# Performance work log

Hardware: AMD Instinct MI355X
Metric: run time of the kernel (lower is better)

## Reference

```python
import jax, jax.numpy as jnp
import numpy as np

B, H, W, C = 8, 64, 64, 512
DQK = C // 8  # query/key channel dim from Conv2D(filters//8, 1)


def setup_inputs() -> dict:
    key = jax.random.key(0)
    ks = jax.random.split(key, 8)
    s_in = 1.0 / np.sqrt(C)
    x = jax.random.normal(ks[0], (B, H, W, C), dtype=jnp.float32)
    Wq = jax.random.normal(ks[1], (C, DQK), dtype=jnp.float32) * s_in
    bq = jnp.zeros((DQK,), dtype=jnp.float32)
    Wk = jax.random.normal(ks[2], (C, DQK), dtype=jnp.float32) * s_in
    bk = jnp.zeros((DQK,), dtype=jnp.float32)
    Wv = jax.random.normal(ks[3], (C, C), dtype=jnp.float32) * s_in
    bv = jnp.zeros((C,), dtype=jnp.float32)
    # gamma initialized to zeros in the original, but use a nonzero value so
    # the attention branch actually contributes to the output/gradients.
    gamma = jnp.ones((1,), dtype=jnp.float32) * 0.5
    return {"x": x, "Wq": Wq, "bq": bq, "Wk": Wk, "bk": bk,
            "Wv": Wv, "bv": bv, "gamma": gamma}


def reference(x, Wq, bq, Wk, bk, Wv, bv, gamma):
    b, h, w, c = x.shape
    n = h * w  # spatial_size
    xf = x.reshape(b, n, c)
    # 1x1 convs == per-pixel channel matmuls
    q = xf @ Wq + bq            # [B, N, C//8]
    k = xf @ Wk + bk            # [B, N, C//8]
    v = xf @ Wv + bv            # [B, N, C]
    # Dot(axes=-1): attn[b,i,j] = sum_d q[b,i,d] * k[b,j,d]
    attn = jnp.einsum('bid,bjd->bij', q, k)
    attn = jax.nn.softmax(attn, axis=-1)
    # Dot(axes=-2): out[b,j,c] = sum_i attn[b,i,j] * v[b,i,c]  (note transpose)
    out = jnp.einsum('bij,bic->bjc', attn, v)
    out = out.reshape(b, h, w, c)
    return gamma * out + x
```

## Files before the change

### kernel.cpp

```cpp
#include <hip/hip_runtime.h>
#include <hip/hip_bf16.h>
#include <cstdio>

typedef unsigned short u16;
typedef __attribute__((ext_vector_type(4))) float f32x4;
typedef __attribute__((ext_vector_type(8))) short s16x8;

#define LOG2E 1.4426950408889634f

__device__ __forceinline__ u16 bf16b(float f) {
  union { float f; unsigned u; } c; c.f = f;
  unsigned u = c.u;
  return (u16)((u + 0x7FFFu + ((u >> 16) & 1u)) >> 16);
}

__device__ __forceinline__ void load16(const void* g, void* l) {
  __builtin_amdgcn_global_load_lds(
      (const __attribute__((address_space(1))) void*)g,
      (__attribute__((address_space(3))) void*)l, 16, 0, 0);
}


__global__ __launch_bounds__(256) void cvt_all_k(const float* __restrict__ x,
                                                 const float* __restrict__ Wq,
                                                 const float* __restrict__ Wk,
                                                 const float* __restrict__ Wv,
                                                 u16* __restrict__ xb,
                                                 u16* __restrict__ Wcat) {
  int bid = blockIdx.x;
  if (bid < 16384) {
    long i = ((long)bid * 256 + threadIdx.x) * 4;
    float4 f = *(const float4*)&x[i];
    unsigned lo = (unsigned)bf16b(f.x) | ((unsigned)bf16b(f.y) << 16);
    unsigned hi = (unsigned)bf16b(f.z) | ((unsigned)bf16b(f.w) << 16);
    uint2 v; v.x = lo; v.y = hi;
    *(uint2*)&xb[i] = v;
  } else {
    int idx = (bid - 16384) * 256 + threadIdx.x;
    int nn = idx >> 9, k = idx & 511;
    float v;
    if (nn < 64)       v = Wq[k * 64 + nn];
    else if (nn < 128) v = Wk[k * 64 + (nn - 64)];
    else               v = Wv[k * 512 + (nn - 128)];
    Wcat[idx] = bf16b(v);
  }
}

__global__ __launch_bounds__(256, 2) void projGemm(
    const u16* __restrict__ A, const u16* __restrict__ B,
    u16* __restrict__ Qb, u16* __restrict__ Kb, u16* __restrict__ Vt,
    const float* __restrict__ bq, const float* __restrict__ bk,
    const float* __restrict__ bv) {
  constexpr int BM = 128, BN = 128, FM = 4, FN = 4;
  __shared__ __align__(16) u16 At[BM * 64];
  __shared__ __align__(16) u16 Bt[BN * 64];
  const int tid = threadIdx.x;
  const int lane = tid & 63, w = tid >> 6;
  const int wr = w >> 1, wc = w & 1;
  const int l15 = lane & 15, lhi = lane >> 4;
  const long m0 = (long)blockIdx.x * BM;
  const long n0 = (long)blockIdx.y * BN;

  f32x4 acc[FM][FN] = {};

  for (int k0 = 0; k0 < 512; k0 += 64) {
#pragma unroll
    for (int it = 0; it < 8; ++it) {
      int q = it * 256 + tid;
      if (q < BM * 8) {
        int row = q >> 3, c8 = q & 7;
        load16(A + (m0 + row) * 512 + k0 + c8 * 8, &At[q * 8]);
      } else {
        int q2 = q - BM * 8;
        int row = q2 >> 3, c8 = q2 & 7;
        load16(B + (n0 + row) * 512 + k0 + c8 * 8, &Bt[q2 * 8]);
      }
    }
    __syncthreads();
#pragma unroll
    for (int kk = 0; kk < 64; kk += 32) {
      s16x8 af[FM], bf[FN];
#pragma unroll
      for (int i = 0; i < FM; ++i)
        af[i] = *(const s16x8*)&At[(wr * 64 + i * 16 + l15) * 64 + kk + lhi * 8];
#pragma unroll
      for (int j = 0; j < FN; ++j)
        bf[j] = *(const s16x8*)&Bt[(wc * 64 + j * 16 + l15) * 64 + kk + lhi * 8];
#pragma unroll
      for (int i = 0; i < FM; ++i)
#pragma unroll
        for (int j = 0; j < FN; ++j)
          acc[i][j] = __builtin_amdgcn_mfma_f32_16x16x32_bf16(af[i], bf[j],
                                                              acc[i][j], 0, 0, 0);
    }
    __syncthreads();
  }

#pragma unroll
  for (int i = 0; i < FM; ++i) {
#pragma unroll
    for (int j = 0; j < FN; ++j) {
      long mm = m0 + wr * 64 + i * 16 + lhi * 4;
      long nn = n0 + wc * 64 + j * 16 + l15;
      if (nn < 64) {
        float bb = bq[nn];
#pragma unroll
        for (int r = 0; r < 4; ++r)
          Qb[(mm + r) * 64 + nn] = bf16b(acc[i][j][r] + bb);
      } else if (nn < 128) {
        float bb = bk[nn - 64];
#pragma unroll
        for (int r = 0; r < 4; ++r)
          Kb[(mm + r) * 64 + nn - 64] = bf16b(acc[i][j][r] + bb);
      } else {
        long c = nn - 128;
        float bb = bv[c];
        unsigned u01 = (unsigned)bf16b(acc[i][j][0] + bb) |
                       ((unsigned)bf16b(acc[i][j][1] + bb) << 16);
        unsigned u23 = (unsigned)bf16b(acc[i][j][2] + bb) |
                       ((unsigned)bf16b(acc[i][j][3] + bb) << 16);
        uint2 u; u.x = u01; u.y = u23;
        *(uint2*)&Vt[(mm >> 12) * 512 * 4096 + c * 4096 + (mm & 4095)] = u;
      }
    }
  }
}

__global__ __launch_bounds__(256, 2) void stats_k(const u16* __restrict__ Qb,
                                                  const u16* __restrict__ Kb,
                                                  float* __restrict__ m_part,
                                                  float* __restrict__ l_part) {
  const int b = blockIdx.z, jc = blockIdx.y;
  const long i0 = (long)blockIdx.x * 128;
  const u16* Q = Qb + (long)b * 4096 * 64;
  const u16* Kp = Kb + (long)b * 4096 * 64;
  __shared__ __align__(16) u16 Qt[128 * 64];
  __shared__ __align__(16) u16 Kt[128 * 64];
  const int tid = threadIdx.x, lane = tid & 63, w = tid >> 6;
  const int l15 = lane & 15, lhi = lane >> 4;

#pragma unroll
  for (int it = 0; it < 4; ++it) {
    int q = it * 256 + tid;
    int row = q >> 3, c8 = q & 7;
    load16(Q + (i0 + row) * 64 + c8 * 8, &Qt[q * 8]);
  }

  float mrun[2][4], lrun[2][4];
#pragma unroll
  for (int i = 0; i < 2; ++i)
#pragma unroll
    for (int r = 0; r < 4; ++r) { mrun[i][r] = -1e30f; lrun[i][r] = 0.f; }

  for (int jt = 0; jt < 8; ++jt) {
    long j0 = (long)jc * 1024 + jt * 128;
#pragma unroll
    for (int it = 0; it < 4; ++it) {
      int q = it * 256 + tid;
      int row = q >> 3, c8 = q & 7;
      load16(Kp + (j0 + row) * 64 + c8 * 8, &Kt[q * 8]);
    }
    __syncthreads();
    f32x4 acc[2][8] = {};
#pragma unroll
    for (int kk = 0; kk < 64; kk += 32) {
      s16x8 af[2], bf[8];
#pragma unroll
      for (int i = 0; i < 2; ++i)
        af[i] = *(const s16x8*)&Qt[(w * 32 + i * 16 + l15) * 64 + kk + lhi * 8];
#pragma unroll
      for (int j = 0; j < 8; ++j)
        bf[j] = *(const s16x8*)&Kt[(j * 16 + l15) * 64 + kk + lhi * 8];
#pragma unroll
      for (int i = 0; i < 2; ++i)
#pragma unroll
        for (int j = 0; j < 8; ++j)
          acc[i][j] = __builtin_amdgcn_mfma_f32_16x16x32_bf16(af[i], bf[j],
                                                              acc[i][j], 0, 0, 0);
    }
#pragma unroll
    for (int i = 0; i < 2; ++i)
#pragma unroll
      for (int r = 0; r < 4; ++r) {
        float tm = acc[i][0][r];
#pragma unroll
        for (int j = 1; j < 8; ++j) tm = fmaxf(tm, acc[i][j][r]);
        float mo = mrun[i][r];
        float mn = fmaxf(mo, tm);
        float s = 0.f;
#pragma unroll
        for (int j = 0; j < 8; ++j) s += __expf(acc[i][j][r] - mn);
        lrun[i][r] = lrun[i][r] * __expf(mo - mn) + s;
        mrun[i][r] = mn;
      }
    __syncthreads();
  }

#pragma unroll
  for (int i = 0; i < 2; ++i)
#pragma unroll
    for (int r = 0; r < 4; ++r) {
      float m = mrun[i][r], l = lrun[i][r];
#pragma unroll
      for (int d = 1; d < 16; d <<= 1) {
        float mo = __shfl_xor(m, d);
        float lo = __shfl_xor(l, d);
        float mn = fmaxf(m, mo);
        l = l * __expf(m - mn) + lo * __expf(mo - mn);
        m = mn;
      }
      if (l15 == 0) {
        long ig = i0 + w * 32 + i * 16 + lhi * 4 + r;
        long idx = ((long)(b * 4 + jc)) * 4096 + ig;
        m_part[idx] = m;
        l_part[idx] = l;
      }
    }
}

__global__ __launch_bounds__(256) void merge_k(const float* __restrict__ m_part,
                                               const float* __restrict__ l_part,
                                               float* __restrict__ mfin) {
  int idx = blockIdx.x * 256 + threadIdx.x;
  int b = idx >> 12, i = idx & 4095;
  float m = -1e30f, l = 0.f;
#pragma unroll
  for (int jc = 0; jc < 4; ++jc) {
    long o = ((long)(b * 4 + jc)) * 4096 + i;
    float mp = m_part[o], lp = l_part[o];
    float mn = fmaxf(m, mp);
    l = l * __expf(m - mn) + lp * __expf(mp - mn);
    m = mn;
  }
  mfin[idx] = fmaf(m, LOG2E, __log2f(l));
}

__global__ __launch_bounds__(256, 2) void fusedPV(
    const u16* __restrict__ Qb, const u16* __restrict__ Kb,
    const u16* __restrict__ Vt, const float* __restrict__ mfin,
    const float* __restrict__ x, const float* __restrict__ gamma,
    float* __restrict__ out) {
  __shared__ __align__(16) u16 Vc[2][256 * 64];
  __shared__ __align__(16) u16 Pl[128 * 64];
  const int tid = threadIdx.x, lane = tid & 63, w = tid >> 6;
  const int l15 = lane & 15, lhi = lane >> 4;
  const int wi = w & 1, wj = w >> 1;
  const int s = blockIdx.x + 32 * (blockIdx.y + 2 * blockIdx.z);
  const int pi = (s & 7) * 64 + (s >> 3);
  const int b = pi >> 6;
  const long c0 = (long)((pi >> 5) & 1) * 256;
  const long j0 = (long)(pi & 31) * 128;
  const u16* Qg = Qb + (long)b * 4096 * 64;
  const u16* Kg = Kb + (long)b * 4096 * 64;
  const u16* Vg = Vt + (long)b * 512 * 4096;
  const float* mg = mfin + (long)b * 4096;
  const float gma = gamma[0];

#pragma unroll
  for (int p = 0; p < 4; ++p) {
    int q = p * 256 + tid;
    int r = q >> 3, col = q & 7, cg = col ^ (r & 7);
    load16(Kg + (j0 + r) * 64 + cg * 8, (char*)Pl + r * 128 + col * 16);
  }
  asm volatile("s_waitcnt vmcnt(0) lgkmcnt(0)\n\ts_barrier" ::: "memory");
  s16x8 kf[4][2];
#pragma unroll
  for (int fj = 0; fj < 4; ++fj)
#pragma unroll
    for (int kx = 0; kx < 2; ++kx) {
      int r = wj * 64 + fj * 16 + l15;
      kf[fj][kx] = *(const s16x8*)((const char*)Pl + r * 128 +
                                   (((kx * 32 + lhi * 8) * 2) ^ ((r & 7) << 4)));
    }
  __syncthreads();

#pragma unroll
  for (int p = 0; p < 8; ++p) {
    int q = p * 256 + tid;
    int r = q >> 3, col = q & 7, cg = col ^ (r & 7);
    load16(Vg + (c0 + r) * 4096 + cg * 8, (char*)&Vc[0][0] + r * 128 + col * 16);
  }

  f32x4 acc2[4][8] = {};
  int cur = 0;

  for (int t = 0; t < 64; ++t) {
    const int i_base = t * 64;
    s16x8 qf[2][2];
#pragma unroll
    for (int fi = 0; fi < 2; ++fi)
#pragma unroll
      for (int kx = 0; kx < 2; ++kx)
        qf[fi][kx] = *(const s16x8*)&Qg[(long)(i_base + wi * 32 + fi * 16 +
                                               l15) * 64 + kx * 32 + lhi * 8];
    asm volatile("s_waitcnt vmcnt(4) lgkmcnt(0)\n\ts_barrier" ::: "memory");
#pragma unroll
    for (int fi = 0; fi < 2; ++fi) {
      f32x4 a1[4] = {};
#pragma unroll
      for (int kx = 0; kx < 2; ++kx)
#pragma unroll
        for (int fj = 0; fj < 4; ++fj)
          a1[fj] = __builtin_amdgcn_mfma_f32_16x16x32_bf16(qf[fi][kx],
                                                           kf[fj][kx], a1[fj],
                                                           0, 0, 0);
      const int i0l = wi * 32 + fi * 16 + lhi * 4;
      f32x4 mv = *(const f32x4*)&mg[i_base + i0l];
#pragma unroll
      for (int fj = 0; fj < 4; ++fj) {
        int j = wj * 64 + fj * 16 + l15;
        float p0 = __builtin_amdgcn_exp2f(fmaf(a1[fj][0], LOG2E, -mv[0]));
        float p1 = __builtin_amdgcn_exp2f(fmaf(a1[fj][1], LOG2E, -mv[1]));
        float p2 = __builtin_amdgcn_exp2f(fmaf(a1[fj][2], LOG2E, -mv[2]));
        float p3 = __builtin_amdgcn_exp2f(fmaf(a1[fj][3], LOG2E, -mv[3]));
        uint2 u;
        u.x = (unsigned)bf16b(p0) | ((unsigned)bf16b(p1) << 16);
        u.y = (unsigned)bf16b(p2) | ((unsigned)bf16b(p3) << 16);
        *(uint2*)((char*)Pl + j * 128 + ((i0l * 2) ^ ((j & 7) << 4))) = u;
      }
    }
    __builtin_amdgcn_sched_barrier(0);
    if (t < 63) {
      const long ib2 = (long)(t + 1) * 64;
#pragma unroll
      for (int p = 0; p < 8; ++p) {
        int q = p * 256 + tid;
        int r = q >> 3, col = q & 7, cg = col ^ (r & 7);
        load16(Vg + (c0 + r) * 4096 + ib2 + cg * 8,
               (char*)&Vc[cur ^ 1][0] + r * 128 + col * 16);
      }
    }
    asm volatile("s_waitcnt lgkmcnt(0)\n\ts_barrier" ::: "memory");
    __builtin_amdgcn_s_setprio(1);
#pragma unroll
    for (int kx = 0; kx < 2; ++kx) {
      int kk = kx * 32;
      s16x8 pa[4];
#pragma unroll
      for (int fm = 0; fm < 4; ++fm) {
        int r = wj * 64 + fm * 16 + l15;
        pa[fm] = *(const s16x8*)((const char*)Pl + r * 128 +
                                 (((kk + lhi * 8) * 2) ^ ((r & 7) << 4)));
      }
#pragma unroll
      for (int fn = 0; fn < 8; ++fn) {
        int r = wi * 128 + fn * 16 + l15;
        s16x8 vb = *(const s16x8*)((const char*)&Vc[cur][0] + r * 128 +
                                   (((kk + lhi * 8) * 2) ^ ((r & 7) << 4)));
#pragma unroll
        for (int fm = 0; fm < 4; ++fm)
          acc2[fm][fn] = __builtin_amdgcn_mfma_f32_16x16x32_bf16(
              pa[fm], vb, acc2[fm][fn], 0, 0, 0);
      }
    }
    __builtin_amdgcn_s_setprio(0);
    cur ^= 1;
  }

#pragma unroll
  for (int fm = 0; fm < 4; ++fm) {
#pragma unroll
    for (int fn = 0; fn < 8; ++fn) {
      long j = j0 + wj * 64 + fm * 16 + lhi * 4;
      long c = c0 + wi * 128 + fn * 16 + l15;
#pragma unroll
      for (int r = 0; r < 4; ++r) {
        long o = ((long)b * 4096 + j + r) * 512 + c;
        out[o] = gma * acc2[fm][fn][r] + x[o];
      }
    }
  }
}


extern "C" void kernel_launch(void* const* d_in, const int* in_sizes, int n_in,
                              void* d_out, int out_size, void* d_ws,
                              size_t ws_size, hipStream_t stream) {
  const float* x = (const float*)d_in[0];
  const float* Wq = (const float*)d_in[1];
  const float* bq = (const float*)d_in[2];
  const float* Wk = (const float*)d_in[3];
  const float* bk = (const float*)d_in[4];
  const float* Wv = (const float*)d_in[5];
  const float* bv = (const float*)d_in[6];
  const float* gamma = (const float*)d_in[7];
  float* out = (float*)d_out;

  char* ws = (char*)d_ws;
  size_t off = 0;
  auto alloc = [&](size_t bytes) {
    char* p = ws + off;
    off += (bytes + 255) & ~(size_t)255;
    return p;
  };
  u16* xb = (u16*)alloc((size_t)32768 * 512 * 2);
  u16* Wcat = (u16*)alloc((size_t)640 * 512 * 2);
  u16* Qb = (u16*)alloc((size_t)8 * 4096 * 64 * 2);
  u16* Kb = (u16*)alloc((size_t)8 * 4096 * 64 * 2);
  u16* Vt = (u16*)alloc((size_t)8 * 512 * 4096 * 2);
  float* m_part = (float*)alloc((size_t)8 * 4 * 4096 * 4);
  float* l_part = (float*)alloc((size_t)8 * 4 * 4096 * 4);
  float* mfin = (float*)alloc((size_t)8 * 4096 * 4);
  if (off > ws_size) {
    fprintf(stderr, "kernel_launch: ws too small: need %zu have %zu\n", off,
            ws_size);
    return;
  }

  cvt_all_k<<<16384 + 1280, 256, 0, stream>>>(x, Wq, Wk, Wv, xb, Wcat);
  projGemm<<<dim3(256, 5, 1), 256, 0, stream>>>(xb, Wcat, Qb, Kb, Vt, bq, bk,
                                                bv);
  stats_k<<<dim3(32, 4, 8), 256, 0, stream>>>(Qb, Kb, m_part, l_part);
  merge_k<<<128, 256, 0, stream>>>(m_part, l_part, mfin);
  fusedPV<<<dim3(32, 2, 8), 256, 0, stream>>>(Qb, Kb, Vt, mfin, x, gamma,
                                              out);
}
```

Baseline: 295.7 us.

## Cover all 512 channels per block and software-pipeline P computation

```diff
diff --git a/kernel.cpp b/kernel.cpp
--- a/kernel.cpp
+++ b/kernel.cpp
@@ -235,20 +235,20 @@
   mfin[idx] = fmaf(m, LOG2E, __log2f(l));
 }
 
-__global__ __launch_bounds__(256, 2) void fusedPV(
+__global__ __launch_bounds__(512, 2) void fusedPV(
     const u16* __restrict__ Qb, const u16* __restrict__ Kb,
     const u16* __restrict__ Vt, const float* __restrict__ mfin,
     const float* __restrict__ x, const float* __restrict__ gamma,
     float* __restrict__ out) {
-  __shared__ __align__(16) u16 Vc[2][256 * 64];
-  __shared__ __align__(16) u16 Pl[128 * 64];
+  __shared__ __align__(16) u16 Vc[2][512 * 64];
+  __shared__ __align__(16) u16 Pl[2][128 * 64];
   const int tid = threadIdx.x, lane = tid & 63, w = tid >> 6;
   const int l15 = lane & 15, lhi = lane >> 4;
   const int wi = w & 1, wj = w >> 1;
-  const int s = blockIdx.x + 32 * (blockIdx.y + 2 * blockIdx.z);
-  const int pi = (s & 7) * 64 + (s >> 3);
-  const int b = pi >> 6;
-  const long c0 = (long)((pi >> 5) & 1) * 256;
+  const int wjj = w & 1, wcc = w >> 1;
+  const int s = blockIdx.x + 32 * blockIdx.z;
+  const int pi = (s & 7) * 32 + (s >> 3);
+  const int b = pi >> 5;
   const long j0 = (long)(pi & 31) * 128;
   const u16* Qg = Qb + (long)b * 4096 * 64;
   const u16* Kg = Kb + (long)b * 4096 * 64;
@@ -257,96 +257,107 @@
   const float gma = gamma[0];
 
 #pragma unroll
-  for (int p = 0; p < 4; ++p) {
-    int q = p * 256 + tid;
+  for (int p = 0; p < 2; ++p) {
+    int q = p * 512 + tid;
     int r = q >> 3, col = q & 7, cg = col ^ (r & 7);
-    load16(Kg + (j0 + r) * 64 + cg * 8, (char*)Pl + r * 128 + col * 16);
+    load16(Kg + (j0 + r) * 64 + cg * 8,
+           (char*)&Pl[0][0] + r * 128 + col * 16);
   }
   asm volatile("s_waitcnt vmcnt(0) lgkmcnt(0)\n\ts_barrier" ::: "memory");
-  s16x8 kf[4][2];
-#pragma unroll
-  for (int fj = 0; fj < 4; ++fj)
+  s16x8 kf[2][2];
+#pragma unroll
+  for (int fj = 0; fj < 2; ++fj)
 #pragma unroll
     for (int kx = 0; kx < 2; ++kx) {
-      int r = wj * 64 + fj * 16 + l15;
-      kf[fj][kx] = *(const s16x8*)((const char*)Pl + r * 128 +
+      int r = wj * 32 + fj * 16 + l15;
+      kf[fj][kx] = *(const s16x8*)((const char*)&Pl[0][0] + r * 128 +
                                    (((kx * 32 + lhi * 8) * 2) ^ ((r & 7) << 4)));
     }
   __syncthreads();
 
+  f32x4 acc2[4][8] = {};
+  s16x8 qf[2][2];
+  f32x4 mv[2];
+
+#pragma unroll
+  for (int fi = 0; fi < 2; ++fi) {
+#pragma unroll
+    for (int kx = 0; kx < 2; ++kx)
+      qf[fi][kx] = *(const s16x8*)&Qg[(long)(wi * 32 + fi * 16 + l15) * 64 +
+                                      kx * 32 + lhi * 8];
+    mv[fi] = *(const f32x4*)&mg[wi * 32 + fi * 16 + lhi * 4];
+  }
 #pragma unroll
   for (int p = 0; p < 8; ++p) {
-    int q = p * 256 + tid;
+    int q = p * 512 + tid;
     int r = q >> 3, col = q & 7, cg = col ^ (r & 7);
-    load16(Vg + (c0 + r) * 4096 + cg * 8, (char*)&Vc[0][0] + r * 128 + col * 16);
-  }
-
-  f32x4 acc2[4][8] = {};
-  int cur = 0;
+    load16(Vg + (long)r * 4096 + cg * 8,
+           (char*)&Vc[0][0] + r * 128 + col * 16);
+  }
+#pragma unroll
+  for (int fi = 0; fi < 2; ++fi) {
+    f32x4 a1[2] = {};
+#pragma unroll
+    for (int kx = 0; kx < 2; ++kx)
+#pragma unroll
+      for (int fj = 0; fj < 2; ++fj)
+        a1[fj] = __builtin_amdgcn_mfma_f32_16x16x32_bf16(qf[fi][kx],
+                                                         kf[fj][kx], a1[fj],
+                                                         0, 0, 0);
+    const int i0l = wi * 32 + fi * 16 + lhi * 4;
+#pragma unroll
+    for (int fj = 0; fj < 2; ++fj) {
+      int j = wj * 32 + fj * 16 + l15;
+      float p0 = __builtin_amdgcn_exp2f(fmaf(a1[fj][0], LOG2E, -mv[fi][0]));
+      float p1 = __builtin_amdgcn_exp2f(fmaf(a1[fj][1], LOG2E, -mv[fi][1]));
+      float p2 = __builtin_amdgcn_exp2f(fmaf(a1[fj][2], LOG2E, -mv[fi][2]));
+      float p3 = __builtin_amdgcn_exp2f(fmaf(a1[fj][3], LOG2E, -mv[fi][3]));
+      uint2 u;
+      u.x = (unsigned)bf16b(p0) | ((unsigned)bf16b(p1) << 16);
+      u.y = (unsigned)bf16b(p2) | ((unsigned)bf16b(p3) << 16);
+      *(uint2*)((char*)&Pl[0][0] + j * 128 + ((i0l * 2) ^ ((j & 7) << 4))) = u;
+    }
+  }
 
   for (int t = 0; t < 64; ++t) {
-    const int i_base = t * 64;
-    s16x8 qf[2][2];
-#pragma unroll
-    for (int fi = 0; fi < 2; ++fi)
-#pragma unroll
-      for (int kx = 0; kx < 2; ++kx)
-        qf[fi][kx] = *(const s16x8*)&Qg[(long)(i_base + wi * 32 + fi * 16 +
-                                               l15) * 64 + kx * 32 + lhi * 8];
-    asm volatile("s_waitcnt vmcnt(4) lgkmcnt(0)\n\ts_barrier" ::: "memory");
-#pragma unroll
-    for (int fi = 0; fi < 2; ++fi) {
-      f32x4 a1[4] = {};
-#pragma unroll
-      for (int kx = 0; kx < 2; ++kx)
-#pragma unroll
-        for (int fj = 0; fj < 4; ++fj)
-          a1[fj] = __builtin_amdgcn_mfma_f32_16x16x32_bf16(qf[fi][kx],
-                                                           kf[fj][kx], a1[fj],
-                                                           0, 0, 0);
-      const int i0l = wi * 32 + fi * 16 + lhi * 4;
-      f32x4 mv = *(const f32x4*)&mg[i_base + i0l];
-#pragma unroll
-      for (int fj = 0; fj < 4; ++fj) {
-        int j = wj * 64 + fj * 16 + l15;
-        float p0 = __builtin_amdgcn_exp2f(fmaf(a1[fj][0], LOG2E, -mv[0]));
-        float p1 = __builtin_amdgcn_exp2f(fmaf(a1[fj][1], LOG2E, -mv[1]));
-        float p2 = __builtin_amdgcn_exp2f(fmaf(a1[fj][2], LOG2E, -mv[2]));
-        float p3 = __builtin_amdgcn_exp2f(fmaf(a1[fj][3], LOG2E, -mv[3]));
-        uint2 u;
-        u.x = (unsigned)bf16b(p0) | ((unsigned)bf16b(p1) << 16);
-        u.y = (unsigned)bf16b(p2) | ((unsigned)bf16b(p3) << 16);
-        *(uint2*)((char*)Pl + j * 128 + ((i0l * 2) ^ ((j & 7) << 4))) = u;
+    const char* plc = (const char*)&Pl[t & 1][0];
+    char* pln = (char*)&Pl[(t + 1) & 1][0];
+    const char* vcc = (const char*)&Vc[t & 1][0];
+    asm volatile("s_waitcnt vmcnt(0) lgkmcnt(0)\n\ts_barrier" ::: "memory");
+    if (t < 63) {
+      const long i2 = (long)(t + 1) * 64;
+#pragma unroll
+      for (int fi = 0; fi < 2; ++fi) {
+#pragma unroll
+        for (int kx = 0; kx < 2; ++kx)
+          qf[fi][kx] = *(const s16x8*)&Qg[(i2 + wi * 32 + fi * 16 + l15) * 64 +
+                                          kx * 32 + lhi * 8];
+        mv[fi] = *(const f32x4*)&mg[i2 + wi * 32 + fi * 16 + lhi * 4];
+      }
+#pragma unroll
+      for (int p = 0; p < 8; ++p) {
+        int q = p * 512 + tid;
+        int r = q >> 3, col = q & 7, cg = col ^ (r & 7);
+        load16(Vg + (long)r * 4096 + i2 + cg * 8,
+               (char*)&Vc[(t + 1) & 1][0] + r * 128 + col * 16);
       }
     }
     __builtin_amdgcn_sched_barrier(0);
-    if (t < 63) {
-      const long ib2 = (long)(t + 1) * 64;
-#pragma unroll
-      for (int p = 0; p < 8; ++p) {
-        int q = p * 256 + tid;
-        int r = q >> 3, col = q & 7, cg = col ^ (r & 7);
-        load16(Vg + (c0 + r) * 4096 + ib2 + cg * 8,
-               (char*)&Vc[cur ^ 1][0] + r * 128 + col * 16);
-      }
-    }
-    asm volatile("s_waitcnt lgkmcnt(0)\n\ts_barrier" ::: "memory");
     __builtin_amdgcn_s_setprio(1);
 #pragma unroll
     for (int kx = 0; kx < 2; ++kx) {
-      int kk = kx * 32;
       s16x8 pa[4];
 #pragma unroll
       for (int fm = 0; fm < 4; ++fm) {
-        int r = wj * 64 + fm * 16 + l15;
-        pa[fm] = *(const s16x8*)((const char*)Pl + r * 128 +
-                                 (((kk + lhi * 8) * 2) ^ ((r & 7) << 4)));
+        int r = wjj * 64 + fm * 16 + l15;
+        pa[fm] = *(const s16x8*)(plc + r * 128 +
+                                 (((kx * 32 + lhi * 8) * 2) ^ ((r & 7) << 4)));
       }
 #pragma unroll
       for (int fn = 0; fn < 8; ++fn) {
-        int r = wi * 128 + fn * 16 + l15;
-        s16x8 vb = *(const s16x8*)((const char*)&Vc[cur][0] + r * 128 +
-                                   (((kk + lhi * 8) * 2) ^ ((r & 7) << 4)));
+        int r = wcc * 128 + fn * 16 + l15;
+        s16x8 vb = *(const s16x8*)(vcc + r * 128 +
+                                   (((kx * 32 + lhi * 8) * 2) ^ ((r & 7) << 4)));
 #pragma unroll
         for (int fm = 0; fm < 4; ++fm)
           acc2[fm][fn] = __builtin_amdgcn_mfma_f32_16x16x32_bf16(
@@ -354,15 +365,40 @@
       }
     }
     __builtin_amdgcn_s_setprio(0);
-    cur ^= 1;
+    if (t < 63) {
+#pragma unroll
+      for (int fi = 0; fi < 2; ++fi) {
+        f32x4 a1[2] = {};
+#pragma unroll
+        for (int kx = 0; kx < 2; ++kx)
+#pragma unroll
+          for (int fj = 0; fj < 2; ++fj)
+            a1[fj] = __builtin_amdgcn_mfma_f32_16x16x32_bf16(qf[fi][kx],
+                                                             kf[fj][kx],
+                                                             a1[fj], 0, 0, 0);
+        const int i0l = wi * 32 + fi * 16 + lhi * 4;
+#pragma unroll
+        for (int fj = 0; fj < 2; ++fj) {
+          int j = wj * 32 + fj * 16 + l15;
+          float p0 = __builtin_amdgcn_exp2f(fmaf(a1[fj][0], LOG2E, -mv[fi][0]));
+          float p1 = __builtin_amdgcn_exp2f(fmaf(a1[fj][1], LOG2E, -mv[fi][1]));
+          float p2 = __builtin_amdgcn_exp2f(fmaf(a1[fj][2], LOG2E, -mv[fi][2]));
+          float p3 = __builtin_amdgcn_exp2f(fmaf(a1[fj][3], LOG2E, -mv[fi][3]));
+          uint2 u;
+          u.x = (unsigned)bf16b(p0) | ((unsigned)bf16b(p1) << 16);
+          u.y = (unsigned)bf16b(p2) | ((unsigned)bf16b(p3) << 16);
+          *(uint2*)(pln + j * 128 + ((i0l * 2) ^ ((j & 7) << 4))) = u;
+        }
+      }
+    }
   }
 
 #pragma unroll
   for (int fm = 0; fm < 4; ++fm) {
 #pragma unroll
     for (int fn = 0; fn < 8; ++fn) {
-      long j = j0 + wj * 64 + fm * 16 + lhi * 4;
-      long c = c0 + wi * 128 + fn * 16 + l15;
+      long j = j0 + wjj * 64 + fm * 16 + lhi * 4;
+      long c = wcc * 128 + fn * 16 + l15;
 #pragma unroll
       for (int r = 0; r < 4; ++r) {
         long o = ((long)b * 4096 + j + r) * 512 + c;
@@ -412,6 +448,6 @@
                                                 bv);
   stats_k<<<dim3(32, 4, 8), 256, 0, stream>>>(Qb, Kb, m_part, l_part);
   merge_k<<<128, 256, 0, stream>>>(m_part, l_part, mfin);
-  fusedPV<<<dim3(32, 2, 8), 256, 0, stream>>>(Qb, Kb, Vt, mfin, x, gamma,
+  fusedPV<<<dim3(32, 1, 8), 512, 0, stream>>>(Qb, Kb, Vt, mfin, x, gamma,
                                               out);
 }
```

Measured after the change: 290.8 us. Within noise of the previous version (-1.7%).
